# Performance work log

Hardware: AMD Instinct MI355X
Metric: run time of the kernel (lower is better)

Reference implementation:

```python
import jax, jax.numpy as jnp
import numpy as np

D_MODEL = 1024
N_HEAD = 16
D_QKV = 64
INIT_RANGE = 0.02
BOUND = float(np.sqrt(3.0) * INIT_RANGE)
SCALE = 1.0 / D_QKV ** 0.5


def setup_inputs() -> dict:
    key = jax.random.key(0)
    kx, k1, k2, k3, k4 = jax.random.split(key, 5)
    B, T = 4, 2048
    x = jax.random.normal(kx, (B, T, D_MODEL), dtype=jnp.float32)
    half_f = D_MODEL // 2
    half_a = D_QKV // 2
    u = lambda k, shp: jax.random.uniform(k, shp, dtype=jnp.float32, minval=-BOUND, maxval=BOUND)
    w_qkv_c = u(k1, (N_HEAD, half_f, 3, half_a))
    w_qkv_p = u(k2, (N_HEAD, half_f, 3, half_a))
    w_o_c = u(k3, (N_HEAD, half_a, half_f))
    w_o_p = u(k4, (N_HEAD, half_a, half_f))
    return {"x": x, "w_qkv_c": w_qkv_c, "w_qkv_p": w_qkv_p, "w_o_c": w_o_c, "w_o_p": w_o_p}


def reference(x, w_qkv_c, w_qkv_p, w_o_c, w_o_p):
    x_c, x_p = jnp.split(x, 2, axis=-1)  # [B,T,d_model//2] each
    # partitioned QKV projections: [B,H,T,3,a/2]
    qkv_c = jnp.einsum('btf,hfca->bhtca', x_c, w_qkv_c)
    qkv_p = jnp.einsum('btf,hfca->bhtca', x_p, w_qkv_p)
    q_c, k_c, v_c = qkv_c[:, :, :, 0], qkv_c[:, :, :, 1], qkv_c[:, :, :, 2]
    q_p, k_p, v_p = qkv_p[:, :, :, 0], qkv_p[:, :, :, 1], qkv_p[:, :, :, 2]
    q = jnp.concatenate([q_c, q_p], axis=-1) * SCALE  # [B,H,T,d_qkv]
    k = jnp.concatenate([k_c, k_p], axis=-1)
    v = jnp.concatenate([v_c, v_p], axis=-1)
    dots = jnp.einsum('bhqa,bhka->bhqk', q, k)  # [B,H,T,T]
    probs = jax.nn.softmax(dots, axis=-1)
    o = jnp.einsum('bhqk,bhka->bhqa', probs, v)  # [B,H,T,d_qkv]
    o_c, o_p = jnp.split(o, 2, axis=-1)
    out_c = jnp.einsum('bhta,haf->btf', o_c, w_o_c)
    out_p = jnp.einsum('bhta,haf->btf', o_p, w_o_p)
    return (out_c, out_p)
```

## Files before the change

### kernel.cpp

```cpp
#include <hip/hip_runtime.h>


typedef __attribute__((ext_vector_type(8))) short bf16x8;
typedef __attribute__((ext_vector_type(4))) float f32x4;
typedef unsigned short u16;

#define QSCALE 0.18033688011112042f

__device__ __forceinline__ u16 f2bf(float f){
  unsigned u = __builtin_bit_cast(unsigned, f);
  u += 0x7FFFu + ((u >> 16) & 1u);
  return (u16)(u >> 16);
}

__device__ __forceinline__ unsigned cvtpk(float lo, float hi){
  unsigned r;
  asm("v_cvt_pk_bf16_f32 %0, %1, %2" : "=v"(r) : "v"(lo), "v"(hi));
  return r;
}

__device__ __forceinline__ void gload16(const void* g, void* l){
  __builtin_amdgcn_global_load_lds(
    (const __attribute__((address_space(1))) unsigned*)g,
    (__attribute__((address_space(3))) unsigned*)l, 16, 0, 0);
}

__global__ __launch_bounds__(256) void k_prep(const float4* __restrict__ x, u16* __restrict__ xA,
                                              const float* __restrict__ wqc, const float* __restrict__ wqp,
                                              u16* __restrict__ wqt,
                                              const float* __restrict__ woc, const float* __restrict__ wop,
                                              u16* __restrict__ wot){
  const unsigned blk = blockIdx.x;
  if (blk < 8192u){
    unsigned i = blk*256 + threadIdx.x;
    float4 v = x[i];
    unsigned j = i*4;
    unsigned row = j >> 10, col = j & 1023u;
    unsigned tile = row >> 4, li = row & 15u;
    unsigned part = col >> 9, ks = (col >> 5) & 15u, lg = (col >> 3) & 3u, e = col & 7u;
    uint2 pk;
    pk.x = (unsigned)f2bf(v.x) | ((unsigned)f2bf(v.y) << 16);
    pk.y = (unsigned)f2bf(v.z) | ((unsigned)f2bf(v.w) << 16);
    *(uint2*)(xA + (size_t)(((tile*2 + part)*16 + ks)*512) + li*32 + lg*8 + e) = pk;
  } else if (blk < 14336u){
    unsigned i = (blk - 8192u)*256 + threadIdx.x;
    unsigned ph = i / 49152u;
    unsigned r  = i - ph*49152u;
    unsigned ks = r / 3072u;
    unsigned r2 = r - ks*3072u;
    unsigned n  = r2 >> 9;
    unsigned r3 = r2 & 511u;
    unsigned lg = r3 >> 7, li = (r3 >> 3) & 15u, e = r3 & 7u;
    unsigned h = ph & 15u;
    unsigned f = ks*32u + lg*8u + e;
    const float* src = (ph < 16) ? wqc : wqp;
    wqt[i] = f2bf(src[h*49152u + f*96u + (n>>1)*32u + (n&1u)*16u + li]);
  } else {
    unsigned i = (blk - 14336u)*256 + threadIdx.x;
    unsigned e = i & 7u;
    unsigned lane = (i >> 3) & 63u;
    unsigned n  = (i >> 9) & 7u;
    unsigned ks = (i >> 12) & 15u;
    unsigned ft = (i >> 16) & 3u;
    unsigned part = i >> 18;
    unsigned f = ft*128u + n*16u + (lane & 15u);
    unsigned a = (lane >> 4)*8u + e;
    const float* src = part ? wop : woc;
    wot[i] = f2bf(src[ks*16384u + a*512u + f]);
  }
}

__global__ __launch_bounds__(256) void k_qkv(const u16* __restrict__ xA, const u16* __restrict__ wt,
                                             u16* __restrict__ Q, u16* __restrict__ K, u16* __restrict__ VT){
  const int lane = threadIdx.x & 63, wv = threadIdx.x >> 6;
  const int lg = lane >> 4, li = lane & 15;
  const int blk = blockIdx.x;
  const int xcd = blk & 7, idx = blk >> 3;
  const int tt  = (idx >> 5)*8 + xcd;
  const int ph  = idx & 31;
  const int row0 = tt*256 + wv*64;
  const int part = ph >> 4, h = ph & 15;

  f32x4 acc[4][6] = {};
  const u16* wbase = wt + (size_t)ph*49152;
  const unsigned aoff = (unsigned)(li*32 + lg*8);
  #pragma unroll 2
  for (int ks = 0; ks < 16; ++ks){
    bf16x8 a[4], b[6];
    #pragma unroll
    for (int m=0;m<4;++m)
      a[m] = *(const bf16x8*)(xA + (size_t)(((tt*16 + wv*4 + m)*2 + part)*16 + ks)*512 + aoff);
    #pragma unroll
    for (int n=0;n<6;++n)
      b[n] = *(const bf16x8*)(wbase + ks*3072 + n*512 + lane*8);
    #pragma unroll
    for (int m=0;m<4;++m)
      #pragma unroll
      for (int n=0;n<6;++n)
        acc[m][n] = __builtin_amdgcn_mfma_f32_16x16x32_bf16(a[m], b[n], acc[m][n], 0, 0, 0);
  }

  const int b_ = row0 >> 11;
  const int bh = b_*16 + h;
  const int tl0 = (row0 & 2047) + lg*4;
  #pragma unroll
  for (int m=0;m<4;++m){
    #pragma unroll
    for (int n=0;n<6;++n){
      const int c = n >> 1;
      const int af = part*32 + (n & 1)*16 + li;
      if (c == 2){
        uint2 pk;
        pk.x = (unsigned)f2bf(acc[m][n][0]) | ((unsigned)f2bf(acc[m][n][1]) << 16);
        pk.y = (unsigned)f2bf(acc[m][n][2]) | ((unsigned)f2bf(acc[m][n][3]) << 16);
        const int c2 = (m&1)*2 + (lg>>1);
        char* dst = (char*)VT + (size_t)bh*262144
                  + (size_t)(((row0 & 2047) >> 5) + (m>>1))*4096
                  + af*64 + ((c2 ^ (af&3))<<4) + (lg&1)*8;
        *(uint2*)dst = pk;
      } else if (c == 1){
        const unsigned kb = ((unsigned)(af>>5))*512 + ((unsigned)((af>>3)&3))*128 + (unsigned)(af&7);
        #pragma unroll
        for (int r=0;r<4;++r){
          int t = tl0 + m*16 + r;
          K[(size_t)bh*131072 + (t>>5)*2048 + ((t>>4)&1)*1024 + kb + (t&15)*8] = f2bf(acc[m][n][r]);
        }
      } else {
        #pragma unroll
        for (int r=0;r<4;++r){
          int t = tl0 + m*16 + r;
          Q[((size_t)bh*2048 + t)*64 + af] = f2bf(acc[m][n][r] * QSCALE);
        }
      }
    }
  }
}

#define NKT 64
#define PLD 40
__global__ __launch_bounds__(256, 4) void k_attn(const u16* __restrict__ Q, const u16* __restrict__ K,
                                                 const u16* __restrict__ VT, u16* __restrict__ OA){
  __shared__ __align__(16) char smem[28672];
  const int lane = threadIdx.x & 63, w = threadIdx.x >> 6;
  const int lg = lane >> 4, li = lane & 15;
  const int swz = (blockIdx.x & 7)*128 + (blockIdx.x >> 3);
  const int bh = swz >> 4, qt = swz & 15;
  const int q0 = qt*128 + w*32;

  const char* Kfb = (const char*)K + (size_t)bh*262144;
  const char* Vg  = (const char*)VT + (size_t)bh*262144;
  const u16*  Qb  = Q + (size_t)bh*131072;
  u16* pw = (u16*)(smem + 8192) + w*2560;

  const unsigned vsrc = (unsigned)(w*1024 + lane*16);
  const unsigned ldst = (unsigned)(w*1024);
  const unsigned vc   = (unsigned)(((lg) ^ (li&3)) << 4);

  bf16x8 aq[2][2];
  #pragma unroll
  for (int m=0;m<2;++m)
    #pragma unroll
    for (int kd=0;kd<2;++kd)
      aq[m][kd] = *(const bf16x8*)(Qb + (size_t)(q0 + m*16 + li)*64 + kd*32 + lg*8);

  const short one_bf = (short)0x3F80;
  bf16x8 ones = {one_bf,one_bf,one_bf,one_bf,one_bf,one_bf,one_bf,one_bf};

  f32x4 o[2][4] = {};
  f32x4 ls[2] = {};
  bf16x8 ka0_00, ka0_01, ka0_10, ka0_11;
  bf16x8 ka1_00, ka1_01, ka1_10, ka1_11;

#define KLOAD(BANK, KT) { const char* kb_ = Kfb + (size_t)(KT)*4096; \
    ka##BANK##_00 = *(const bf16x8*)(kb_ +        lane*16); \
    ka##BANK##_01 = *(const bf16x8*)(kb_ + 1024 + lane*16); \
    ka##BANK##_10 = *(const bf16x8*)(kb_ + 2048 + lane*16); \
    ka##BANK##_11 = *(const bf16x8*)(kb_ + 3072 + lane*16); }

  auto QKEXP = [&](bf16x8 b00, bf16x8 b01, bf16x8 b10, bf16x8 b11, u16* pW){
    #pragma unroll
    for (int n=0;n<2;++n){
      bf16x8 bk0 = n ? b10 : b00;
      bf16x8 bk1 = n ? b11 : b01;
      #pragma unroll
      for (int m=0;m<2;++m){
        f32x4 s = {0.f,0.f,0.f,0.f};
        s = __builtin_amdgcn_mfma_f32_16x16x32_bf16(bk0, aq[m][0], s, 0, 0, 0);
        s = __builtin_amdgcn_mfma_f32_16x16x32_bf16(bk1, aq[m][1], s, 0, 0, 0);
        uint2 pk;
        pk.x = cvtpk(__builtin_exp2f(s[0]), __builtin_exp2f(s[1]));
        pk.y = cvtpk(__builtin_exp2f(s[2]), __builtin_exp2f(s[3]));
        *(uint2*)(pW + (size_t)(m*16 + li)*PLD + n*16 + lg*4) = pk;
      }
    }
  };
  auto PV = [&](const char* sV, const u16* pR){
    bf16x8 pa0 = *(const bf16x8*)(pR + (size_t)(     li)*PLD + lg*8);
    bf16x8 pa1 = *(const bf16x8*)(pR + (size_t)(16 + li)*PLD + lg*8);
    __builtin_amdgcn_s_setprio(1);
    #pragma unroll
    for (int nd=0;nd<4;++nd){
      bf16x8 bv = *(const bf16x8*)(sV + (nd*16 + li)*64 + vc);
      o[0][nd] = __builtin_amdgcn_mfma_f32_16x16x32_bf16(pa0, bv, o[0][nd], 0, 0, 0);
      o[1][nd] = __builtin_amdgcn_mfma_f32_16x16x32_bf16(pa1, bv, o[1][nd], 0, 0, 0);
    }
    ls[0] = __builtin_amdgcn_mfma_f32_16x16x32_bf16(pa0, ones, ls[0], 0, 0, 0);
    ls[1] = __builtin_amdgcn_mfma_f32_16x16x32_bf16(pa1, ones, ls[1], 0, 0, 0);
    __builtin_amdgcn_s_setprio(0);
  };

#define AITER(KT, PR, PN) { \
    gload16(Vg + (size_t)((KT)+1)*4096u + vsrc, smem + (PN)*4096 + ldst); \
    if ((KT) + 2 < NKT) KLOAD(PR, (KT)+2); \
    QKEXP(ka##PN##_00, ka##PN##_01, ka##PN##_10, ka##PN##_11, pw + (PN)*1280); \
    PV(smem + (PR)*4096, pw + (PR)*1280); \
    asm volatile("s_waitcnt vmcnt(0)" ::: "memory"); \
    __builtin_amdgcn_s_barrier(); }

  gload16(Vg + vsrc, smem + ldst);
  KLOAD(0, 0);
  KLOAD(1, 1);
  asm volatile("s_waitcnt vmcnt(0)" ::: "memory");
  __builtin_amdgcn_s_barrier();
  QKEXP(ka0_00, ka0_01, ka0_10, ka0_11, pw);
  __builtin_amdgcn_s_barrier();

  for (int base = 0; base < NKT-2; base += 2){
    AITER(base,   0, 1);
    AITER(base+1, 1, 0);
  }
  AITER(NKT-2, 0, 1);
  PV(smem + 4096, pw + 1280);

  const int b_ = bh >> 4, h = bh & 15;
  #pragma unroll
  for (int m=0;m<2;++m){
    const int tile = (b_*2048 + q0 + m*16) >> 4;
    #pragma unroll
    for (int r=0;r<4;++r){
      float linv = 1.0f / ls[m][r];
      #pragma unroll
      for (int nd=0;nd<4;++nd){
        OA[(size_t)(((tile*16 + h)*2 + (nd>>1))*512)
           + (lg*4 + r)*32 + ((nd&1)*2 + (li>>3))*8 + (li&7)] = f2bf(o[m][nd][r] * linv);
      }
    }
  }
#undef AITER
#undef KLOAD
}

__global__ __launch_bounds__(256) void k_proj(const u16* __restrict__ OA, const u16* __restrict__ wot,
                                              float* __restrict__ out){
  const int lane = threadIdx.x & 63, wv = threadIdx.x >> 6;
  const int lg = lane >> 4, li = lane & 15;
  const int blk = blockIdx.x;
  const int xcd = blk & 7, idx = blk >> 3;
  const int rowTile = (idx >> 3)*8 + xcd;
  const int colTile = idx & 7;
  const int row0 = rowTile*128 + wv*32;
  const int part = colTile >> 2;
  const int ft   = colTile & 3;
  const int f0   = ft*128;

  f32x4 acc[2][8] = {};
  const u16* wbase = wot + (size_t)part*262144 + (size_t)ft*65536;
  const unsigned aoff = (unsigned)(li*32 + lg*8);
  #pragma unroll 4
  for (int ks = 0; ks < 16; ++ks){
    bf16x8 a[2];
    #pragma unroll
    for (int m=0;m<2;++m)
      a[m] = *(const bf16x8*)(OA + (size_t)((((rowTile*8 + wv*2 + m)*16 + ks)*2 + part)*512) + aoff);
    #pragma unroll
    for (int n=0;n<8;++n){
      bf16x8 b = *(const bf16x8*)(wbase + ks*4096 + n*512 + lane*8);
      #pragma unroll
      for (int m=0;m<2;++m)
        acc[m][n] = __builtin_amdgcn_mfma_f32_16x16x32_bf16(a[m], b, acc[m][n], 0, 0, 0);
    }
  }
  float* obp = out + (size_t)part*(8192u*512u);
  #pragma unroll
  for (int m=0;m<2;++m)
    #pragma unroll
    for (int n=0;n<8;++n)
      #pragma unroll
      for (int r=0;r<4;++r)
        obp[(size_t)(row0 + m*16 + lg*4 + r)*512 + f0 + n*16 + li] = acc[m][n][r];
}

extern "C" void kernel_launch(void* const* d_in, const int* in_sizes, int n_in,
                              void* d_out, int out_size, void* d_ws, size_t ws_size,
                              hipStream_t stream){
  const float* x   = (const float*)d_in[0];
  const float* wqc = (const float*)d_in[1];
  const float* wqp = (const float*)d_in[2];
  const float* woc = (const float*)d_in[3];
  const float* wop = (const float*)d_in[4];

  char* ws = (char*)d_ws;
  u16* xA  = (u16*)(ws);
  u16* Q   = (u16*)(ws + 16777216);
  u16* K   = (u16*)(ws + 2*16777216);
  u16* VT  = (u16*)(ws + 3*16777216);
  u16* wqt = (u16*)(ws + 4*16777216);
  u16* wot = (u16*)(ws + 4*16777216 + 3145728);
  u16* OA  = xA;
  float* out = (float*)d_out;

  k_prep <<<16384, 256, 0, stream>>>((const float4*)x, xA, wqc, wqp, wqt, woc, wop, wot);
  k_qkv  <<<1024,  256, 0, stream>>>(xA, wqt, Q, K, VT);
  k_attn <<<1024,  256, 0, stream>>>(Q, K, VT, OA);
  k_proj <<<512,   256, 0, stream>>>(OA, wot, out);
}
```

Baseline: 171.3 us.

## Load V directly into registers in MFMA fragment layout, drop LDS staging and barriers

```diff
diff --git a/kernel.cpp b/kernel.cpp
--- a/kernel.cpp
+++ b/kernel.cpp
@@ -17,12 +17,6 @@
   unsigned r;
   asm("v_cvt_pk_bf16_f32 %0, %1, %2" : "=v"(r) : "v"(lo), "v"(hi));
   return r;
-}
-
-__device__ __forceinline__ void gload16(const void* g, void* l){
-  __builtin_amdgcn_global_load_lds(
-    (const __attribute__((address_space(1))) unsigned*)g,
-    (__attribute__((address_space(3))) unsigned*)l, 16, 0, 0);
 }
 
 __global__ __launch_bounds__(256) void k_prep(const float4* __restrict__ x, u16* __restrict__ xA,
@@ -113,10 +107,9 @@
         uint2 pk;
         pk.x = (unsigned)f2bf(acc[m][n][0]) | ((unsigned)f2bf(acc[m][n][1]) << 16);
         pk.y = (unsigned)f2bf(acc[m][n][2]) | ((unsigned)f2bf(acc[m][n][3]) << 16);
-        const int c2 = (m&1)*2 + (lg>>1);
-        char* dst = (char*)VT + (size_t)bh*262144
-                  + (size_t)(((row0 & 2047) >> 5) + (m>>1))*4096
-                  + af*64 + ((c2 ^ (af&3))<<4) + (lg&1)*8;
+        const int kt = ((row0 & 2047) >> 5) + (m>>1);
+        u16* dst = VT + (size_t)bh*131072 + (size_t)kt*2048
+                 + (part*2 + (n&1))*512 + ((m&1)*2 + (lg>>1))*128 + li*8 + (lg&1)*4;
         *(uint2*)dst = pk;
       } else if (c == 1){
         const unsigned kb = ((unsigned)(af>>5))*512 + ((unsigned)((af>>3)&3))*128 + (unsigned)(af&7);
@@ -140,7 +133,7 @@
 #define PLD 40
 __global__ __launch_bounds__(256, 4) void k_attn(const u16* __restrict__ Q, const u16* __restrict__ K,
                                                  const u16* __restrict__ VT, u16* __restrict__ OA){
-  __shared__ __align__(16) char smem[28672];
+  __shared__ __align__(16) char smem[20480];
   const int lane = threadIdx.x & 63, w = threadIdx.x >> 6;
   const int lg = lane >> 4, li = lane & 15;
   const int swz = (blockIdx.x & 7)*128 + (blockIdx.x >> 3);
@@ -148,13 +141,9 @@
   const int q0 = qt*128 + w*32;
 
   const char* Kfb = (const char*)K + (size_t)bh*262144;
-  const char* Vg  = (const char*)VT + (size_t)bh*262144;
+  const char* Vfb = (const char*)VT + (size_t)bh*262144;
   const u16*  Qb  = Q + (size_t)bh*131072;
-  u16* pw = (u16*)(smem + 8192) + w*2560;
-
-  const unsigned vsrc = (unsigned)(w*1024 + lane*16);
-  const unsigned ldst = (unsigned)(w*1024);
-  const unsigned vc   = (unsigned)(((lg) ^ (li&3)) << 4);
+  u16* pw = (u16*)smem + w*2560;
 
   bf16x8 aq[2][2];
   #pragma unroll
@@ -170,12 +159,18 @@
   f32x4 ls[2] = {};
   bf16x8 ka0_00, ka0_01, ka0_10, ka0_11;
   bf16x8 ka1_00, ka1_01, ka1_10, ka1_11;
+  bf16x8 va_0, va_1, va_2, va_3;
 
 #define KLOAD(BANK, KT) { const char* kb_ = Kfb + (size_t)(KT)*4096; \
     ka##BANK##_00 = *(const bf16x8*)(kb_ +        lane*16); \
     ka##BANK##_01 = *(const bf16x8*)(kb_ + 1024 + lane*16); \
     ka##BANK##_10 = *(const bf16x8*)(kb_ + 2048 + lane*16); \
     ka##BANK##_11 = *(const bf16x8*)(kb_ + 3072 + lane*16); }
+#define VLOAD(KT) { const char* vb_ = Vfb + (size_t)(KT)*4096; \
+    va_0 = *(const bf16x8*)(vb_ +        lane*16); \
+    va_1 = *(const bf16x8*)(vb_ + 1024 + lane*16); \
+    va_2 = *(const bf16x8*)(vb_ + 2048 + lane*16); \
+    va_3 = *(const bf16x8*)(vb_ + 3072 + lane*16); }
 
   auto QKEXP = [&](bf16x8 b00, bf16x8 b01, bf16x8 b10, bf16x8 b11, u16* pW){
     #pragma unroll
@@ -194,43 +189,40 @@
       }
     }
   };
-  auto PV = [&](const char* sV, const u16* pR){
+  auto PV = [&](const u16* pR){
     bf16x8 pa0 = *(const bf16x8*)(pR + (size_t)(     li)*PLD + lg*8);
     bf16x8 pa1 = *(const bf16x8*)(pR + (size_t)(16 + li)*PLD + lg*8);
     __builtin_amdgcn_s_setprio(1);
-    #pragma unroll
-    for (int nd=0;nd<4;++nd){
-      bf16x8 bv = *(const bf16x8*)(sV + (nd*16 + li)*64 + vc);
-      o[0][nd] = __builtin_amdgcn_mfma_f32_16x16x32_bf16(pa0, bv, o[0][nd], 0, 0, 0);
-      o[1][nd] = __builtin_amdgcn_mfma_f32_16x16x32_bf16(pa1, bv, o[1][nd], 0, 0, 0);
-    }
+    o[0][0] = __builtin_amdgcn_mfma_f32_16x16x32_bf16(pa0, va_0, o[0][0], 0, 0, 0);
+    o[1][0] = __builtin_amdgcn_mfma_f32_16x16x32_bf16(pa1, va_0, o[1][0], 0, 0, 0);
+    o[0][1] = __builtin_amdgcn_mfma_f32_16x16x32_bf16(pa0, va_1, o[0][1], 0, 0, 0);
+    o[1][1] = __builtin_amdgcn_mfma_f32_16x16x32_bf16(pa1, va_1, o[1][1], 0, 0, 0);
+    o[0][2] = __builtin_amdgcn_mfma_f32_16x16x32_bf16(pa0, va_2, o[0][2], 0, 0, 0);
+    o[1][2] = __builtin_amdgcn_mfma_f32_16x16x32_bf16(pa1, va_2, o[1][2], 0, 0, 0);
+    o[0][3] = __builtin_amdgcn_mfma_f32_16x16x32_bf16(pa0, va_3, o[0][3], 0, 0, 0);
+    o[1][3] = __builtin_amdgcn_mfma_f32_16x16x32_bf16(pa1, va_3, o[1][3], 0, 0, 0);
     ls[0] = __builtin_amdgcn_mfma_f32_16x16x32_bf16(pa0, ones, ls[0], 0, 0, 0);
     ls[1] = __builtin_amdgcn_mfma_f32_16x16x32_bf16(pa1, ones, ls[1], 0, 0, 0);
     __builtin_amdgcn_s_setprio(0);
   };
 
 #define AITER(KT, PR, PN) { \
-    gload16(Vg + (size_t)((KT)+1)*4096u + vsrc, smem + (PN)*4096 + ldst); \
     if ((KT) + 2 < NKT) KLOAD(PR, (KT)+2); \
     QKEXP(ka##PN##_00, ka##PN##_01, ka##PN##_10, ka##PN##_11, pw + (PN)*1280); \
-    PV(smem + (PR)*4096, pw + (PR)*1280); \
-    asm volatile("s_waitcnt vmcnt(0)" ::: "memory"); \
-    __builtin_amdgcn_s_barrier(); }
-
-  gload16(Vg + vsrc, smem + ldst);
+    PV(pw + (PR)*1280); \
+    if ((KT) + 1 < NKT) VLOAD((KT)+1); }
+
   KLOAD(0, 0);
   KLOAD(1, 1);
-  asm volatile("s_waitcnt vmcnt(0)" ::: "memory");
-  __builtin_amdgcn_s_barrier();
+  VLOAD(0);
   QKEXP(ka0_00, ka0_01, ka0_10, ka0_11, pw);
-  __builtin_amdgcn_s_barrier();
 
   for (int base = 0; base < NKT-2; base += 2){
     AITER(base,   0, 1);
     AITER(base+1, 1, 0);
   }
   AITER(NKT-2, 0, 1);
-  PV(smem + 4096, pw + 1280);
+  PV(pw + 1280);
 
   const int b_ = bh >> 4, h = bh & 15;
   #pragma unroll
@@ -248,6 +240,7 @@
   }
 #undef AITER
 #undef KLOAD
+#undef VLOAD
 }
 
 __global__ __launch_bounds__(256) void k_proj(const u16* __restrict__ OA, const u16* __restrict__ wot,
```

New measurement: 168.4 us. Within noise of the previous version (-1.7%).
